# Optimization experiments

Measured on AMD Instinct MI355X. Metric: run time of the kernel, lower is better.

## Reference

```python
import jax, jax.numpy as jnp
import numpy as np

D_MODEL = 4096
N_TYPES = 6  # fixed event_types list in the module


def setup_inputs() -> dict:
    key = jax.random.key(0)
    ks = jax.random.split(key, 7)
    E, B, d = 131072, 16384, D_MODEL
    return {
        "event_type": jax.random.randint(ks[0], (E,), 0, N_TYPES),
        "confidence": jax.random.uniform(ks[1], (E,), jnp.float32),
        "location": jax.random.uniform(ks[2], (E, 2), jnp.float32) * jnp.array([640.0, 480.0], jnp.float32),
        "batch_idx": jax.random.randint(ks[3], (E,), 0, B),
        "batch_size": B,
        "type_emb": jax.random.normal(ks[4], (N_TYPES, d // 4), jnp.float32),
        "W1": jax.random.normal(ks[5], (d // 2, d // 4 + 3), jnp.float32) / np.sqrt(d // 4 + 3).astype(np.float32),
        "b1": jnp.zeros((d // 2,), jnp.float32),
        "W2": jax.random.normal(ks[6], (d, d // 2), jnp.float32) / np.sqrt(d // 2).astype(np.float32),
        "b2": jnp.zeros((d,), jnp.float32),
    }


def reference(event_type, confidence, location, batch_idx, batch_size, type_emb, W1, b1, W2, b2):
    E = confidence.shape[0]
    B = batch_size
    # per-batch-slot max confidence (empty slots -> -inf)
    seg_max = jax.ops.segment_max(confidence, batch_idx, num_segments=B)
    is_top = confidence == seg_max[batch_idx]
    # first event attaining the max (matches torch's max-over-list semantics)
    cand = jnp.where(is_top, jnp.arange(E), E)
    top_idx = jnp.full((B,), E, dtype=cand.dtype).at[batch_idx].min(cand)
    has_event = top_idx < E
    safe_idx = jnp.where(has_event, top_idx, 0)

    emb = type_emb[event_type[safe_idx]]                 # [B, d/4]
    c = confidence[safe_idx][:, None]                    # [B, 1]
    loc = location[safe_idx] / jnp.array([640.0, 480.0], jnp.float32)  # [B, 2]
    feats = jnp.concatenate([emb, c, loc], axis=-1)      # [B, d/4 + 3]

    h = jax.nn.relu(feats @ W1.T + b1)                   # [B, d/2]
    out = h @ W2.T + b2                                  # [B, d]
    return jnp.where(has_event[:, None], out, jnp.zeros((), out.dtype))
```

## Files before the change

kernel.cpp:

```cpp
#include <hip/hip_runtime.h>
#include <hip/hip_bf16.h>

#define NT 6
#define BM 256
#define BN 256
#define BK 32
#define SLOT 16384

typedef __attribute__((ext_vector_type(4))) float f32x4;
typedef __attribute__((ext_vector_type(8))) short bf16x8;

__device__ __forceinline__ short f2bf(float f) {
    __hip_bfloat16 h = __float2bfloat16(f);
    return (short)__builtin_bit_cast(unsigned short, h);
}

__global__ void k_segmax(const float* __restrict__ conf,
                         const int* __restrict__ bidx,
                         unsigned long long* __restrict__ packed, int E) {
    int i = blockIdx.x * blockDim.x + threadIdx.x;
    if (i >= E) return;
    unsigned cb = __float_as_uint(conf[i]);
    unsigned long long p = ((unsigned long long)cb << 32) | (unsigned)(~(unsigned)i);
    atomicMax(&packed[bidx[i]], p);
}

__global__ void k_base(const float* __restrict__ emb, const float* __restrict__ W1,
                       const float* __restrict__ b1, float* __restrict__ base,
                       float* __restrict__ vecs, int d2, int d4) {
    int gw = (blockIdx.x * blockDim.x + threadIdx.x) >> 6;
    int lane = threadIdx.x & 63;
    int t = gw / d2, n = gw % d2;
    const float* e = emb + (size_t)t * d4;
    const float* w = W1 + (size_t)n * (d4 + 3);
    float s = 0.f;
    for (int k = lane; k < d4; k += 64) s += e[k] * w[k];
#pragma unroll
    for (int m = 32; m; m >>= 1) s += __shfl_xor(s, m);
    if (lane == 0) {
        base[gw] = s + b1[n];
        if (t == 0) {
            vecs[n]          = w[d4];
            vecs[d2 + n]     = w[d4 + 1];
            vecs[2 * d2 + n] = w[d4 + 2];
        }
    }
}

__global__ void k_w2cast(const float* __restrict__ W2, short* __restrict__ W2b, long n) {
    long i = ((long)blockIdx.x * blockDim.x + threadIdx.x) * 8;
    if (i >= n) return;
    bf16x8 v;
#pragma unroll
    for (int j = 0; j < 8; ++j) v[j] = f2bf(W2[i + j]);
    *(bf16x8*)(W2b + i) = v;
}

__global__ void k_h(const unsigned long long* __restrict__ packed,
                    const int* __restrict__ etype, const float* __restrict__ loc,
                    const float* __restrict__ base, const float* __restrict__ vecs,
                    float* __restrict__ mask, short* __restrict__ h, int d2) {
    int b = blockIdx.x;
    int tid = threadIdx.x;
    unsigned long long p = packed[b];
    bool has = (p != 0ULL);
    float conf = 0.f, lx = 0.f, ly = 0.f;
    int t = 0;
    if (has) {
        unsigned idx = ~(unsigned)(p & 0xFFFFFFFFu);
        conf = __uint_as_float((unsigned)(p >> 32));
        t  = etype[idx];
        lx = loc[2 * (size_t)idx]     * (1.0f / 640.0f);
        ly = loc[2 * (size_t)idx + 1] * (1.0f / 480.0f);
    }
    if (tid == 0) mask[b] = has ? 1.0f : 0.0f;
    const float* bs = base + (size_t)t * d2;
    const float* cv = vecs;
    const float* xv = vecs + d2;
    const float* yv = vecs + 2 * d2;
    int n0 = tid * 8;
    bf16x8 v;
#pragma unroll
    for (int j = 0; j < 8; ++j) {
        int n = n0 + j;
        float g = bs[n] + conf * cv[n] + lx * xv[n] + ly * yv[n];
        g = fmaxf(g, 0.f);
        v[j] = has ? f2bf(g) : (short)0;
    }
    *(bf16x8*)(h + (size_t)b * d2 + n0) = v;
}


#define GLL(src, dst) __builtin_amdgcn_global_load_lds(                      \
    (const __attribute__((address_space(1))) void*)(src),                    \
    (__attribute__((address_space(3))) void*)(dst), 16, 0, 0)

#define SB __builtin_amdgcn_sched_barrier(0)

__global__ __launch_bounds__(512, 2)
void k_gemm(const short* __restrict__ A, const short* __restrict__ Bm,
            const float* __restrict__ b2, const float* __restrict__ mask,
            float* __restrict__ C, int M, int N, int K, int nbn) {
    __shared__ __align__(16) short lds[4 * SLOT];

    int tid = threadIdx.x;
    int lane = tid & 63;
    int wave = tid >> 6;
    int wr = wave >> 2, wc = wave & 3;

    int bid = blockIdx.x;
    int wg = (bid & 7) * ((int)gridDim.x >> 3) + (bid >> 3);
    int bm = wg / nbn, bn = wg % nbn;
    int row0 = bm * BM, col0 = bn * BN;

    int srow = tid >> 2;
    int chunkL = (tid & 3) ^ ((srow >> 1) & 3);
    const short* pa0 = A + (size_t)(row0 + srow) * K + chunkL * 8;
    const short* pa1 = pa0 + (size_t)128 * K;
    const short* pb0 = Bm + (size_t)(col0 + srow) * K + chunkL * 8;
    const short* pb1 = pb0 + (size_t)128 * K;
    int dA0 = tid * 8, dA1 = 4096 + tid * 8;
    int dB0 = 8192 + tid * 8, dB1 = 12288 + tid * 8;

    int frow = lane & 15, fk = lane >> 4;
    int cp = fk ^ ((frow >> 1) & 3);
    int aoff = (wr * 128 + frow) * 32 + cp * 8;
    int boff = 8192 + (wc * 64 + frow) * 32 + cp * 8;

    f32x4 acc[8][4] = {};
    bf16x8 a03[4], a47[4], bv[4];

    int KT = K / BK;

    {
        short* s0 = lds + 0 * SLOT;
        GLL(pa0, s0 + dA0); GLL(pa1, s0 + dA1); GLL(pb0, s0 + dB0); GLL(pb1, s0 + dB1);
        pa0 += BK; pa1 += BK; pb0 += BK; pb1 += BK;
        short* s1 = lds + 1 * SLOT;
        GLL(pa0, s1 + dA0); GLL(pa1, s1 + dA1); GLL(pb0, s1 + dB0); GLL(pb1, s1 + dB1);
        pa0 += BK; pa1 += BK; pb0 += BK; pb1 += BK;
        short* s2 = lds + 2 * SLOT;
        GLL(pa0, s2 + dA0); GLL(pa1, s2 + dA1); GLL(pb0, s2 + dB0); GLL(pb1, s2 + dB1);
        pa0 += BK; pa1 += BK; pb0 += BK; pb1 += BK;
    }
    asm volatile("s_waitcnt vmcnt(8)" ::: "memory");
    __builtin_amdgcn_s_barrier();

#pragma unroll 1
    for (int t = 0; t < KT; ++t) {
        const short* sr = lds + (t & 3) * SLOT;
        short* sw = lds + ((t + 3) & 3) * SLOT;
        bool stage = (t < KT - 3);

#pragma unroll
        for (int n = 0; n < 4; ++n)
            bv[n] = *(const bf16x8*)(sr + boff + n * 512);
#pragma unroll
        for (int m = 0; m < 4; ++m)
            a03[m] = *(const bf16x8*)(sr + aoff + m * 512);
        if (stage) { GLL(pa0, sw + dA0); GLL(pa1, sw + dA1); }
        SB;
        __builtin_amdgcn_s_barrier();
        asm volatile("s_waitcnt lgkmcnt(0)" ::: "memory");
        SB;
        __builtin_amdgcn_s_setprio(1);
#pragma unroll
        for (int m = 0; m < 4; ++m)
#pragma unroll
            for (int n = 0; n < 4; ++n)
                acc[m][n] = __builtin_amdgcn_mfma_f32_16x16x32_bf16(
                    a03[m], bv[n], acc[m][n], 0, 0, 0);
        __builtin_amdgcn_s_setprio(0);
        SB;
        __builtin_amdgcn_s_barrier();

#pragma unroll
        for (int m = 0; m < 4; ++m)
            a47[m] = *(const bf16x8*)(sr + aoff + 2048 + m * 512);
        if (stage) { GLL(pb0, sw + dB0); GLL(pb1, sw + dB1); }
        pa0 += BK; pa1 += BK; pb0 += BK; pb1 += BK;
        SB;
        __builtin_amdgcn_s_barrier();
        asm volatile("s_waitcnt lgkmcnt(0)" ::: "memory");
        SB;
        __builtin_amdgcn_s_setprio(1);
#pragma unroll
        for (int m = 0; m < 4; ++m)
#pragma unroll
            for (int n = 0; n < 4; ++n)
                acc[4 + m][n] = __builtin_amdgcn_mfma_f32_16x16x32_bf16(
                    a47[m], bv[n], acc[4 + m][n], 0, 0, 0);
        __builtin_amdgcn_s_setprio(0);
        SB;
        if (t < KT - 1) {
            if (t < KT - 3)       asm volatile("s_waitcnt vmcnt(8)" ::: "memory");
            else if (t == KT - 3) asm volatile("s_waitcnt vmcnt(4)" ::: "memory");
            else                  asm volatile("s_waitcnt vmcnt(0)" ::: "memory");
            __builtin_amdgcn_s_barrier();
        }
    }

#pragma unroll
    for (int m = 0; m < 8; ++m) {
        int rbase = row0 + wr * 128 + m * 16 + (lane >> 4) * 4;
#pragma unroll
        for (int j = 0; j < 4; ++j) {
            int r = rbase + j;
            float mk = mask[r];
#pragma unroll
            for (int n = 0; n < 4; ++n) {
                int c = col0 + wc * 64 + n * 16 + frow;
                C[(size_t)r * N + c] = (acc[m][n][j] + b2[c]) * mk;
            }
        }
    }
}

extern "C" void kernel_launch(void* const* d_in, const int* in_sizes, int n_in,
                              void* d_out, int out_size, void* d_ws, size_t ws_size,
                              hipStream_t stream) {
    const int* etype   = (const int*)d_in[0];
    const float* conf  = (const float*)d_in[1];
    const float* loc   = (const float*)d_in[2];
    const int* bidx    = (const int*)d_in[3];
    const float* emb   = (const float*)d_in[5];
    const float* W1    = (const float*)d_in[6];
    const float* b1    = (const float*)d_in[7];
    const float* W2    = (const float*)d_in[8];
    const float* b2    = (const float*)d_in[9];
    float* out = (float*)d_out;

    int E  = in_sizes[0];
    int d2 = in_sizes[7];
    int d  = in_sizes[9];
    int d4 = in_sizes[5] / NT;
    int B  = out_size / d;

    char* ws = (char*)d_ws;
    unsigned long long* packed = (unsigned long long*)ws;
    float* mask = (float*)(ws + (size_t)B * 8);
    float* base = mask + B;
    float* vecs = base + NT * d2;
    short* w2b  = (short*)(vecs + 3 * d2);
    short* h    = w2b + (size_t)d * d2;

    hipMemsetAsync(packed, 0, (size_t)B * 8, stream);
    k_segmax<<<(E + 255) / 256, 256, 0, stream>>>(conf, bidx, packed, E);
    k_base<<<(NT * d2) / 4, 256, 0, stream>>>(emb, W1, b1, base, vecs, d2, d4);
    long nw2 = (long)d * d2;
    k_w2cast<<<(int)(nw2 / 8 / 256), 256, 0, stream>>>(W2, w2b, nw2);
    k_h<<<B, 256, 0, stream>>>(packed, etype, loc, base, vecs, mask, h, d2);
    int nbm = B / BM, nbn = d / BN;
    k_gemm<<<dim3(nbm * nbn), dim3(512), 0, stream>>>(h, w2b, b2, mask, out, B, d, d2, nbn);
}
```

Before: 326.7 us.

## Restructure GEMM main loop to BK=64 double buffer with half-tile staged loads

The bf16 GEMM main loop moves from a 4-stage BK=32 ring buffer to a 2-stage BK=64 double buffer. Each stage is split into A and B halves that are loaded asynchronously and interleaved with four MFMA quadrants. Each warp's output tile changes from contiguous 128x64 to a split layout of two 64-row by two 32-column pieces, and the LDS swizzle changes to XOR over 8 chunks. The aim is fewer barriers per unit of K and better overlap of global-to-LDS loads with MFMA work, at the cost of shallower prefetch depth and more complex vmcnt bookkeeping.

```diff
diff --git a/kernel.cpp b/kernel.cpp
--- a/kernel.cpp
+++ b/kernel.cpp
@@ -4,8 +4,11 @@
 #define NT 6
 #define BM 256
 #define BN 256
-#define BK 32
-#define SLOT 16384
+#define BK 64
+#define SLOT_S 32768
+#define AH1 8192
+#define BH0 16384
+#define BH1 24576
 
 typedef __attribute__((ext_vector_type(4))) float f32x4;
 typedef __attribute__((ext_vector_type(8))) short bf16x8;
@@ -97,11 +100,29 @@
 
 #define SB __builtin_amdgcn_sched_barrier(0)
 
+#define ST_AH0(ws, kt) { GLL(pA + (size_t)(kt) * 64, (ws) + dst1);           \
+                         GLL(pA + (size_t)64 * K + (kt) * 64, (ws) + dst2); }
+#define ST_AH1(ws, kt) { GLL(pA + (size_t)128 * K + (kt) * 64, (ws) + AH1 + dst1); \
+                         GLL(pA + (size_t)192 * K + (kt) * 64, (ws) + AH1 + dst2); }
+#define ST_BH0(ws, kt) { GLL(pB + (size_t)(kt) * 64, (ws) + BH0 + dst1);     \
+                         GLL(pB + (size_t)64 * K + (kt) * 64, (ws) + BH0 + dst2); }
+#define ST_BH1(ws, kt) { GLL(pB + (size_t)128 * K + (kt) * 64, (ws) + BH1 + dst1); \
+                         GLL(pB + (size_t)192 * K + (kt) * 64, (ws) + BH1 + dst2); }
+
+#define MFMA16(AI, NI, BVV)                                                  \
+    _Pragma("unroll") for (int m = 0; m < 4; ++m)                            \
+    _Pragma("unroll") for (int n = 0; n < 2; ++n) {                          \
+        acc[(AI) + m][(NI) + n] = __builtin_amdgcn_mfma_f32_16x16x32_bf16(   \
+            aA[m][0], BVV[n][0], acc[(AI) + m][(NI) + n], 0, 0, 0);          \
+        acc[(AI) + m][(NI) + n] = __builtin_amdgcn_mfma_f32_16x16x32_bf16(   \
+            aA[m][1], BVV[n][1], acc[(AI) + m][(NI) + n], 0, 0, 0);          \
+    }
+
 __global__ __launch_bounds__(512, 2)
 void k_gemm(const short* __restrict__ A, const short* __restrict__ Bm,
             const float* __restrict__ b2, const float* __restrict__ mask,
             float* __restrict__ C, int M, int N, int K, int nbn) {
-    __shared__ __align__(16) short lds[4 * SLOT];
+    __shared__ __align__(16) short lds[2 * SLOT_S];
 
     int tid = threadIdx.x;
     int lane = tid & 63;
@@ -113,104 +134,115 @@
     int bm = wg / nbn, bn = wg % nbn;
     int row0 = bm * BM, col0 = bn * BN;
 
-    int srow = tid >> 2;
-    int chunkL = (tid & 3) ^ ((srow >> 1) & 3);
-    const short* pa0 = A + (size_t)(row0 + srow) * K + chunkL * 8;
-    const short* pa1 = pa0 + (size_t)128 * K;
-    const short* pb0 = Bm + (size_t)(col0 + srow) * K + chunkL * 8;
-    const short* pb1 = pb0 + (size_t)128 * K;
-    int dA0 = tid * 8, dA1 = 4096 + tid * 8;
-    int dB0 = 8192 + tid * 8, dB1 = 12288 + tid * 8;
+    int r1 = tid >> 3;
+    int pg = tid & 7;
+    int cg = pg ^ (r1 & 7);
+    const short* pA = A + (size_t)(row0 + r1) * K + cg * 8;
+    const short* pB = Bm + (size_t)(col0 + r1) * K + cg * 8;
+    int dst1 = tid * 8;
+    int dst2 = 4096 + tid * 8;
 
     int frow = lane & 15, fk = lane >> 4;
-    int cp = fk ^ ((frow >> 1) & 3);
-    int aoff = (wr * 128 + frow) * 32 + cp * 8;
-    int boff = 8192 + (wc * 64 + frow) * 32 + cp * 8;
+    int kx = frow & 7;
+    int aoffs0 = (wr * 64 + frow) * 64 + ((fk) ^ kx) * 8;
+    int aoffs1 = (wr * 64 + frow) * 64 + ((4 + fk) ^ kx) * 8;
+    int boffs0 = (wc * 32 + frow) * 64 + ((fk) ^ kx) * 8;
+    int boffs1 = (wc * 32 + frow) * 64 + ((4 + fk) ^ kx) * 8;
 
     f32x4 acc[8][4] = {};
-    bf16x8 a03[4], a47[4], bv[4];
+    bf16x8 aA[4][2], bB0[2][2], bB1[2][2];
 
     int KT = K / BK;
 
-    {
-        short* s0 = lds + 0 * SLOT;
-        GLL(pa0, s0 + dA0); GLL(pa1, s0 + dA1); GLL(pb0, s0 + dB0); GLL(pb1, s0 + dB1);
-        pa0 += BK; pa1 += BK; pb0 += BK; pb1 += BK;
-        short* s1 = lds + 1 * SLOT;
-        GLL(pa0, s1 + dA0); GLL(pa1, s1 + dA1); GLL(pb0, s1 + dB0); GLL(pb1, s1 + dB1);
-        pa0 += BK; pa1 += BK; pb0 += BK; pb1 += BK;
-        short* s2 = lds + 2 * SLOT;
-        GLL(pa0, s2 + dA0); GLL(pa1, s2 + dA1); GLL(pb0, s2 + dB0); GLL(pb1, s2 + dB1);
-        pa0 += BK; pa1 += BK; pb0 += BK; pb1 += BK;
-    }
-    asm volatile("s_waitcnt vmcnt(8)" ::: "memory");
+    ST_AH0(lds, 0); ST_BH0(lds, 0); ST_BH1(lds, 0); ST_AH1(lds, 0);
+    asm volatile("s_waitcnt vmcnt(0)" ::: "memory");
     __builtin_amdgcn_s_barrier();
+    SB;
 
 #pragma unroll 1
     for (int t = 0; t < KT; ++t) {
-        const short* sr = lds + (t & 3) * SLOT;
-        short* sw = lds + ((t + 3) & 3) * SLOT;
-        bool stage = (t < KT - 3);
-
-#pragma unroll
-        for (int n = 0; n < 4; ++n)
-            bv[n] = *(const bf16x8*)(sr + boff + n * 512);
-#pragma unroll
-        for (int m = 0; m < 4; ++m)
-            a03[m] = *(const bf16x8*)(sr + aoff + m * 512);
-        if (stage) { GLL(pa0, sw + dA0); GLL(pa1, sw + dA1); }
+        const short* sl = lds + (t & 1) * SLOT_S;
+        short* wsl = lds + ((t + 1) & 1) * SLOT_S;
+        bool stg = (t < KT - 1);
+
+#pragma unroll
+        for (int n = 0; n < 2; ++n) {
+            bB0[n][0] = *(const bf16x8*)(sl + BH0 + boffs0 + n * 1024);
+            bB0[n][1] = *(const bf16x8*)(sl + BH0 + boffs1 + n * 1024);
+        }
+#pragma unroll
+        for (int m = 0; m < 4; ++m) {
+            aA[m][0] = *(const bf16x8*)(sl + aoffs0 + m * 1024);
+            aA[m][1] = *(const bf16x8*)(sl + aoffs1 + m * 1024);
+        }
+        if (stg) { ST_AH0(wsl, t + 1); ST_BH0(wsl, t + 1); }
         SB;
         __builtin_amdgcn_s_barrier();
         asm volatile("s_waitcnt lgkmcnt(0)" ::: "memory");
         SB;
         __builtin_amdgcn_s_setprio(1);
-#pragma unroll
-        for (int m = 0; m < 4; ++m)
-#pragma unroll
-            for (int n = 0; n < 4; ++n)
-                acc[m][n] = __builtin_amdgcn_mfma_f32_16x16x32_bf16(
-                    a03[m], bv[n], acc[m][n], 0, 0, 0);
-        __builtin_amdgcn_s_setprio(0);
-        SB;
-        __builtin_amdgcn_s_barrier();
-
-#pragma unroll
-        for (int m = 0; m < 4; ++m)
-            a47[m] = *(const bf16x8*)(sr + aoff + 2048 + m * 512);
-        if (stage) { GLL(pb0, sw + dB0); GLL(pb1, sw + dB1); }
-        pa0 += BK; pa1 += BK; pb0 += BK; pb1 += BK;
+        MFMA16(0, 0, bB0)
+        __builtin_amdgcn_s_setprio(0);
+        SB;
+        if (stg) asm volatile("s_waitcnt vmcnt(6)" ::: "memory");
+        else     asm volatile("s_waitcnt vmcnt(2)" ::: "memory");
+        __builtin_amdgcn_s_barrier();
+
+#pragma unroll
+        for (int n = 0; n < 2; ++n) {
+            bB1[n][0] = *(const bf16x8*)(sl + BH1 + boffs0 + n * 1024);
+            bB1[n][1] = *(const bf16x8*)(sl + BH1 + boffs1 + n * 1024);
+        }
+        if (stg) ST_BH1(wsl, t + 1);
         SB;
         __builtin_amdgcn_s_barrier();
         asm volatile("s_waitcnt lgkmcnt(0)" ::: "memory");
         SB;
         __builtin_amdgcn_s_setprio(1);
-#pragma unroll
-        for (int m = 0; m < 4; ++m)
-#pragma unroll
-            for (int n = 0; n < 4; ++n)
-                acc[4 + m][n] = __builtin_amdgcn_mfma_f32_16x16x32_bf16(
-                    a47[m], bv[n], acc[4 + m][n], 0, 0, 0);
-        __builtin_amdgcn_s_setprio(0);
-        SB;
-        if (t < KT - 1) {
-            if (t < KT - 3)       asm volatile("s_waitcnt vmcnt(8)" ::: "memory");
-            else if (t == KT - 3) asm volatile("s_waitcnt vmcnt(4)" ::: "memory");
-            else                  asm volatile("s_waitcnt vmcnt(0)" ::: "memory");
+        MFMA16(0, 2, bB1)
+        __builtin_amdgcn_s_setprio(0);
+        SB;
+        if (stg) asm volatile("s_waitcnt vmcnt(6)" ::: "memory");
+        else     asm volatile("s_waitcnt vmcnt(0)" ::: "memory");
+        __builtin_amdgcn_s_barrier();
+
+#pragma unroll
+        for (int m = 0; m < 4; ++m) {
+            aA[m][0] = *(const bf16x8*)(sl + AH1 + aoffs0 + m * 1024);
+            aA[m][1] = *(const bf16x8*)(sl + AH1 + aoffs1 + m * 1024);
+        }
+        if (stg) ST_AH1(wsl, t + 1);
+        SB;
+        __builtin_amdgcn_s_barrier();
+        asm volatile("s_waitcnt lgkmcnt(0)" ::: "memory");
+        SB;
+        __builtin_amdgcn_s_setprio(1);
+        MFMA16(4, 2, bB1)
+        __builtin_amdgcn_s_setprio(0);
+        SB;
+
+        __builtin_amdgcn_s_setprio(1);
+        MFMA16(4, 0, bB0)
+        __builtin_amdgcn_s_setprio(0);
+        SB;
+        if (stg) {
+            asm volatile("s_waitcnt vmcnt(4)" ::: "memory");
             __builtin_amdgcn_s_barrier();
-        }
-    }
-
-#pragma unroll
-    for (int m = 0; m < 8; ++m) {
-        int rbase = row0 + wr * 128 + m * 16 + (lane >> 4) * 4;
+            SB;
+        }
+    }
+
+#pragma unroll
+    for (int mi = 0; mi < 8; ++mi) {
+        int rbase = row0 + (mi >> 2) * 128 + wr * 64 + (mi & 3) * 16 + fk * 4;
 #pragma unroll
         for (int j = 0; j < 4; ++j) {
             int r = rbase + j;
             float mk = mask[r];
 #pragma unroll
-            for (int n = 0; n < 4; ++n) {
-                int c = col0 + wc * 64 + n * 16 + frow;
-                C[(size_t)r * N + c] = (acc[m][n][j] + b2[c]) * mk;
+            for (int ni = 0; ni < 4; ++ni) {
+                int cc = col0 + (ni >> 1) * 128 + wc * 32 + (ni & 1) * 16 + frow;
+                C[(size_t)r * N + cc] = (acc[mi][ni][j] + b2[cc]) * mk;
             }
         }
     }
```

Measured after the change: 307.4 us. -5.9%, faster.
